# Performance work log

Hardware: AMD Instinct MI355X
Metric: run time of the kernel (lower is better)

## Reference

```python
import jax, jax.numpy as jnp
import numpy as np

N_NODES = 100000


def _graph_conv(x, W, b, src, dst, deg_out, deg_in, relu):
    # DGL GraphConv, norm='both':
    #   h = (x * D_out^{-1/2}) W ; agg = scatter_sum over edges ; out = agg * D_in^{-1/2} + b
    norm_src = jax.lax.rsqrt(jnp.maximum(deg_out, 1.0))  # [N]
    norm_dst = jax.lax.rsqrt(jnp.maximum(deg_in, 1.0))   # [N]
    h = (x * norm_src[:, None]) @ W                       # [N, d_out]
    agg = jax.ops.segment_sum(h[src], dst, num_segments=N_NODES)  # [N, d_out]
    out = agg * norm_dst[:, None] + b
    return jax.nn.relu(out) if relu else out


def setup_inputs() -> dict:
    key = jax.random.key(0)
    ks = jax.random.split(key, 8)
    E = 1600000
    in_dim, hid_dim, out_dim = 128, 128, 64
    feat = jax.random.normal(ks[0], (N_NODES, in_dim), dtype=jnp.float32)
    edge_index = jax.random.randint(ks[1], (2, E), 0, N_NODES, dtype=jnp.int64)
    s = 1.0 / np.sqrt(in_dim)
    sh = 1.0 / np.sqrt(hid_dim)
    return {
        "feat": feat,
        "edge_index": edge_index,
        "W0": jax.random.normal(ks[2], (in_dim, hid_dim), dtype=jnp.float32) * s,
        "b0": jnp.zeros((hid_dim,), dtype=jnp.float32),
        "W1": jax.random.normal(ks[3], (hid_dim, hid_dim), dtype=jnp.float32) * sh,
        "b1": jnp.zeros((hid_dim,), dtype=jnp.float32),
        "W2": jax.random.normal(ks[4], (hid_dim, out_dim), dtype=jnp.float32) * sh,
        "b2": jnp.zeros((out_dim,), dtype=jnp.float32),
    }


def reference(feat, edge_index, W0, b0, W1, b1, W2, b2):
    src, dst = edge_index[0], edge_index[1]
    ones = jnp.ones(src.shape, dtype=feat.dtype)
    deg_out = jax.ops.segment_sum(ones, src, num_segments=N_NODES)  # src out-degree
    deg_in = jax.ops.segment_sum(ones, dst, num_segments=N_NODES)   # dst in-degree
    h = _graph_conv(feat, W0, b0, src, dst, deg_out, deg_in, relu=True)
    h = _graph_conv(h, W1, b1, src, dst, deg_out, deg_in, relu=True)
    h = _graph_conv(h, W2, b2, src, dst, deg_out, deg_in, relu=False)
    return h
```

## Files before the change

kernel.cpp:

```cpp
#include <hip/hip_runtime.h>
#include <hip/hip_fp16.h>


typedef _Float16 h8 __attribute__((ext_vector_type(8)));
typedef float f32x4 __attribute__((ext_vector_type(4)));

#define HWORDS 25024
#define NHIST 32

__global__ __launch_bounds__(256) void k_pre(const int* __restrict__ src, int E,
                                             unsigned* __restrict__ histo,
                                             int* __restrict__ deg_i, int n,
                                             const float* __restrict__ W0,
                                             const float* __restrict__ W1,
                                             const float* __restrict__ W2,
                                             __half* __restrict__ Wt0,
                                             __half* __restrict__ Wt1,
                                             __half* __restrict__ Wt2) {
    __shared__ unsigned H[HWORDS];
    const int b = blockIdx.x;
    if (b < NHIST) {
        for (int i = threadIdx.x; i < HWORDS; i += 256) H[i] = 0;
        __syncthreads();
        const int perB = ((E + NHIST - 1) / NHIST + 3) & ~3;
        const int e0 = b * perB, e1 = min(e0 + perB, E);
        int i = e0 + threadIdx.x * 4;
        for (; i + 3 < e1; i += 1024) {
            int4 s4 = *(const int4*)(src + i);
            atomicAdd(&H[s4.x >> 2], 1u << ((s4.x & 3) * 8));
            atomicAdd(&H[s4.y >> 2], 1u << ((s4.y & 3) * 8));
            atomicAdd(&H[s4.z >> 2], 1u << ((s4.z & 3) * 8));
            atomicAdd(&H[s4.w >> 2], 1u << ((s4.w & 3) * 8));
        }
        for (; i < e1; ++i) {
            int s = src[i];
            atomicAdd(&H[s >> 2], 1u << ((s & 3) * 8));
        }
        __syncthreads();
        unsigned* outp = histo + b * HWORDS;
        for (int i2 = threadIdx.x; i2 < HWORDS; i2 += 256) outp[i2] = H[i2];
    } else if (b < NHIST + 8) {
        int per = (n + 7) / 8;
        int s0 = (b - NHIST) * per, s1 = min(s0 + per, n);
        for (int i = s0 + threadIdx.x; i < s1; i += 256) deg_i[i] = 0;
    } else {
        int j0 = (b - NHIST - 8) * 20480;
        for (int j = j0 + threadIdx.x; j < j0 + 20480; j += 256) {
            if (j < 16384) {
                int nn = j >> 7, k = j & 127;
                Wt0[j] = __float2half(W0[k * 128 + nn]);
            } else if (j < 32768) {
                int i2 = j - 16384;
                int nn = i2 >> 7, k = i2 & 127;
                Wt1[i2] = __float2half(W1[k * 128 + nn]);
            } else if (j < 40960) {
                int i2 = j - 32768;
                int nn = i2 >> 7, k = i2 & 127;
                Wt2[i2] = __float2half(W2[k * 64 + nn]);
            }
        }
    }
}

template <int BN, bool F32A>
__device__ __forceinline__ void gemm_body(const void* __restrict__ Ap,
                                          const __half* __restrict__ Wt,
                                          __half* __restrict__ C, int n, int gb) {
    constexpr int K = 128, BM = 128, LDR = K + 8;
    __shared__ __half Al[BM * LDR];
    __shared__ __half Bl[BN * LDR];
    const int tid = threadIdx.x;
    const int row0 = gb * BM;
    if (F32A) {
        const float* A = (const float*)Ap;
#pragma unroll
        for (int q = 0; q < 16; ++q) {
            int fi = q * 256 + tid;
            int r = fi >> 5, c = (fi & 31) * 4;
            int gr = row0 + r;
            float4 v = make_float4(0.f, 0.f, 0.f, 0.f);
            if (gr < n) v = *(const float4*)(A + (size_t)gr * K + c);
            __half2 h0 = __floats2half2_rn(v.x, v.y);
            __half2 h1 = __floats2half2_rn(v.z, v.w);
            uint2 pk = make_uint2(*(unsigned*)&h0, *(unsigned*)&h1);
            *(uint2*)&Al[r * LDR + c] = pk;
        }
    } else {
        const __half* A = (const __half*)Ap;
#pragma unroll
        for (int q = 0; q < 8; ++q) {
            int fi = q * 256 + tid;
            int r = fi >> 4, c = (fi & 15) * 8;
            int gr = row0 + r;
            float4 v = make_float4(0.f, 0.f, 0.f, 0.f);
            if (gr < n) v = *(const float4*)(A + (size_t)gr * K + c);
            *(float4*)&Al[r * LDR + c] = v;
        }
    }
#pragma unroll
    for (int q = 0; q < BN / 16; ++q) {
        int fi = q * 256 + tid;
        int r = fi >> 4, c = (fi & 15) * 8;
        *(float4*)&Bl[r * LDR + c] = *(const float4*)(Wt + (size_t)r * K + c);
    }
    __syncthreads();
    const int wid = tid >> 6, lane = tid & 63;
    const int lo = lane & 15, hi = lane >> 4;
    constexpr int NC = BN / 16;
    f32x4 acc[2][NC];
#pragma unroll
    for (int t = 0; t < 2; ++t)
#pragma unroll
        for (int c = 0; c < NC; ++c) acc[t][c] = (f32x4){0.f, 0.f, 0.f, 0.f};
#pragma unroll
    for (int kc = 0; kc < 4; ++kc) {
        h8 aF[2];
#pragma unroll
        for (int t = 0; t < 2; ++t)
            aF[t] = *(const h8*)&Al[(32 * wid + 16 * t + lo) * LDR + 32 * kc + 8 * hi];
#pragma unroll
        for (int c = 0; c < NC; ++c) {
            h8 bF = *(const h8*)&Bl[(16 * c + lo) * LDR + 32 * kc + 8 * hi];
#pragma unroll
            for (int t = 0; t < 2; ++t)
                acc[t][c] = __builtin_amdgcn_mfma_f32_16x16x32_f16(aF[t], bF, acc[t][c], 0, 0, 0);
        }
    }
#pragma unroll
    for (int t = 0; t < 2; ++t) {
#pragma unroll
        for (int j = 0; j < 4; ++j) {
            int gr = row0 + 32 * wid + 16 * t + 4 * hi + j;
            if (gr < n) {
#pragma unroll
                for (int c = 0; c < NC; ++c)
                    C[(size_t)gr * BN + 16 * c + lo] = __float2half(acc[t][c][j]);
            }
        }
    }
}

__global__ __launch_bounds__(256) void k_fused0(
        const float* __restrict__ feat, const __half* __restrict__ Wt0,
        __half* __restrict__ Hu, int n,
        const int* __restrict__ dst, int E,
        int* __restrict__ deg_i, int* __restrict__ pos,
        int CB, int T) {
    const int b = blockIdx.x;
    const long lo = (long)b * CB / T, hi = (long)(b + 1) * CB / T;
    if (hi > lo) {
        int i = (int)lo * 256 + threadIdx.x;
        const int stride = CB * 256;
        for (; i < E; i += stride) {
            pos[i] = atomicAdd(&deg_i[dst[i]], 1);
        }
    } else {
        gemm_body<128, true>(feat, Wt0, Hu, n, b - (int)lo);
    }
}

template <int BN>
__global__ __launch_bounds__(256) void k_gemm(const __half* __restrict__ X,
                                              const __half* __restrict__ Wt,
                                              __half* __restrict__ C, int n) {
    gemm_body<BN, false>(X, Wt, C, n, blockIdx.x);
}

__global__ __launch_bounds__(256) void k_scan1(const int* __restrict__ deg_i,
                                               const unsigned* __restrict__ histo,
                                               int* __restrict__ rp,
                                               int* __restrict__ bsum,
                                               float* __restrict__ ns,
                                               float* __restrict__ nd, int n) {
    const int tid = threadIdx.x, lane = tid & 63, wid = tid >> 6;
    int i = blockIdx.x * 256 + tid;
    int v = (i < n) ? deg_i[i] : 0;
    if (i < n) {
        nd[i] = rsqrtf((float)max(v, 1));
        int w = i >> 2, sh = (i & 3) * 8;
        int dgo = 0;
#pragma unroll
        for (int b = 0; b < NHIST; ++b)
            dgo += (histo[b * HWORDS + w] >> sh) & 255u;
        ns[i] = rsqrtf((float)max(dgo, 1));
    }
    int x = v;
#pragma unroll
    for (int off = 1; off < 64; off <<= 1) {
        int t = __shfl_up(x, off, 64);
        if (lane >= off) x += t;
    }
    __shared__ int ws[4];
    if (lane == 63) ws[wid] = x;
    __syncthreads();
    int wo = 0;
    for (int k = 0; k < wid; ++k) wo += ws[k];
    int incl = wo + x;
    if (i < n) rp[i] = incl - v;
    if (tid == 255) bsum[blockIdx.x] = incl;
}

__global__ __launch_bounds__(512) void k_scan2(int* __restrict__ bsum, int nb,
                                               int* __restrict__ rpN) {
    __shared__ int s[512];
    const int tid = threadIdx.x;
    int v = (tid < nb) ? bsum[tid] : 0;
    s[tid] = v;
    __syncthreads();
    for (int off = 1; off < 512; off <<= 1) {
        int t = (tid >= off) ? s[tid - off] : 0;
        __syncthreads();
        s[tid] += t;
        __syncthreads();
    }
    if (tid < nb) bsum[tid] = s[tid] - v;
    if (tid == nb - 1) *rpN = v;
}

__global__ void k_scatter(const int* __restrict__ src, const int* __restrict__ dst, int E,
                          const int* __restrict__ rp, const int* __restrict__ bsum,
                          const int* __restrict__ pos, int* __restrict__ csr) {
    int i = blockIdx.x * blockDim.x + threadIdx.x;
    int stride = gridDim.x * blockDim.x;
    for (; i < E; i += stride) {
        int d = dst[i];
        csr[rp[d] + bsum[d >> 8] + pos[i]] = src[i];
    }
}

template <bool RELU, bool SSCALE>
__global__ __launch_bounds__(256) void k_agg128h(const __half2* __restrict__ H,
                                                 const int* __restrict__ rp,
                                                 const int* __restrict__ bsum,
                                                 const int* __restrict__ cs,
                                                 const float* __restrict__ nd,
                                                 const float* __restrict__ ns,
                                                 const float* __restrict__ b,
                                                 __half2* __restrict__ out, int n) {
    const int wid = threadIdx.x >> 6, lane = threadIdx.x & 63;
    const int node = blockIdx.x * 4 + wid;
    if (node >= n) return;
    const int beg = rp[node] + bsum[node >> 8];
    const int end = rp[node + 1] + bsum[(node + 1) >> 8];
    float2 a0 = make_float2(0.f, 0.f), a1 = a0, a2 = a0, a3 = a0;
    float2 a4 = a0, a5 = a0, a6 = a0, a7 = a0;
    for (int e = beg; e < end; e += 8) {
        int s[8];
        float w[8];
#pragma unroll
        for (int j = 0; j < 8; ++j) {
            int idx = e + j;
            int r = (idx < end) ? idx : beg;
            r = __builtin_amdgcn_readfirstlane(r);
            s[j] = cs[r];
            w[j] = (idx < end) ? 1.f : 0.f;
        }
        if (SSCALE) {
#pragma unroll
            for (int j = 0; j < 8; ++j) w[j] *= ns[s[j]];
        }
        float2 v0 = __half22float2(H[(size_t)s[0] * 64 + lane]);
        float2 v1 = __half22float2(H[(size_t)s[1] * 64 + lane]);
        float2 v2 = __half22float2(H[(size_t)s[2] * 64 + lane]);
        float2 v3 = __half22float2(H[(size_t)s[3] * 64 + lane]);
        float2 v4 = __half22float2(H[(size_t)s[4] * 64 + lane]);
        float2 v5 = __half22float2(H[(size_t)s[5] * 64 + lane]);
        float2 v6 = __half22float2(H[(size_t)s[6] * 64 + lane]);
        float2 v7 = __half22float2(H[(size_t)s[7] * 64 + lane]);
        a0.x = fmaf(v0.x, w[0], a0.x); a0.y = fmaf(v0.y, w[0], a0.y);
        a1.x = fmaf(v1.x, w[1], a1.x); a1.y = fmaf(v1.y, w[1], a1.y);
        a2.x = fmaf(v2.x, w[2], a2.x); a2.y = fmaf(v2.y, w[2], a2.y);
        a3.x = fmaf(v3.x, w[3], a3.x); a3.y = fmaf(v3.y, w[3], a3.y);
        a4.x = fmaf(v4.x, w[4], a4.x); a4.y = fmaf(v4.y, w[4], a4.y);
        a5.x = fmaf(v5.x, w[5], a5.x); a5.y = fmaf(v5.y, w[5], a5.y);
        a6.x = fmaf(v6.x, w[6], a6.x); a6.y = fmaf(v6.y, w[6], a6.y);
        a7.x = fmaf(v7.x, w[7], a7.x); a7.y = fmaf(v7.y, w[7], a7.y);
    }
    const float sc = nd[node];
    const float sn = ns[node];
    float2 bb = ((const float2*)b)[lane];
    float ax = ((a0.x + a1.x) + (a2.x + a3.x)) + ((a4.x + a5.x) + (a6.x + a7.x));
    float ay = ((a0.y + a1.y) + (a2.y + a3.y)) + ((a4.y + a5.y) + (a6.y + a7.y));
    float ox = ax * sc + bb.x;
    float oy = ay * sc + bb.y;
    if (RELU) { ox = fmaxf(ox, 0.f); oy = fmaxf(oy, 0.f); }
    ox *= sn; oy *= sn;
    out[(size_t)node * 64 + lane] = __floats2half2_rn(ox, oy);
}

__global__ __launch_bounds__(256) void k_agg64h(const __half* __restrict__ H,
                                                const int* __restrict__ rp,
                                                const int* __restrict__ bsum,
                                                const int* __restrict__ cs,
                                                const float* __restrict__ nd,
                                                const float* __restrict__ b,
                                                float* __restrict__ out, int n) {
    const int wid = threadIdx.x >> 6, lane = threadIdx.x & 63;
    const int node = blockIdx.x * 4 + wid;
    if (node >= n) return;
    const int beg = rp[node] + bsum[node >> 8];
    const int end = rp[node + 1] + bsum[(node + 1) >> 8];
    float a0 = 0.f, a1 = 0.f, a2 = 0.f, a3 = 0.f;
    float a4 = 0.f, a5 = 0.f, a6 = 0.f, a7 = 0.f;
    for (int e = beg; e < end; e += 8) {
        int s[8];
        float w[8];
#pragma unroll
        for (int j = 0; j < 8; ++j) {
            int idx = e + j;
            int r = (idx < end) ? idx : beg;
            r = __builtin_amdgcn_readfirstlane(r);
            s[j] = cs[r];
            w[j] = (idx < end) ? 1.f : 0.f;
        }
        a0 = fmaf(__half2float(H[(size_t)s[0] * 64 + lane]), w[0], a0);
        a1 = fmaf(__half2float(H[(size_t)s[1] * 64 + lane]), w[1], a1);
        a2 = fmaf(__half2float(H[(size_t)s[2] * 64 + lane]), w[2], a2);
        a3 = fmaf(__half2float(H[(size_t)s[3] * 64 + lane]), w[3], a3);
        a4 = fmaf(__half2float(H[(size_t)s[4] * 64 + lane]), w[4], a4);
        a5 = fmaf(__half2float(H[(size_t)s[5] * 64 + lane]), w[5], a5);
        a6 = fmaf(__half2float(H[(size_t)s[6] * 64 + lane]), w[6], a6);
        a7 = fmaf(__half2float(H[(size_t)s[7] * 64 + lane]), w[7], a7);
    }
    float a = ((a0 + a1) + (a2 + a3)) + ((a4 + a5) + (a6 + a7));
    out[(size_t)node * 64 + lane] = a * nd[node] + b[lane];
}

extern "C" void kernel_launch(void* const* d_in, const int* in_sizes, int n_in,
                              void* d_out, int out_size, void* d_ws, size_t ws_size,
                              hipStream_t stream) {
    const float* feat = (const float*)d_in[0];
    const int* ei = (const int*)d_in[1];
    const float* W0 = (const float*)d_in[2];
    const float* b0 = (const float*)d_in[3];
    const float* W1 = (const float*)d_in[4];
    const float* b1 = (const float*)d_in[5];
    const float* W2 = (const float*)d_in[6];
    const float* b2 = (const float*)d_in[7];
    float* out = (float*)d_out;

    const int N = in_sizes[0] / 128;
    const int E = in_sizes[1] / 2;
    const int* src = ei;
    const int* dst = ei + E;
    const int NB = (N + 255) / 256;

    char* w = (char*)d_ws;
    float* norm_src = (float*)w; w += (size_t)N * 4;
    float* norm_dst = (float*)w; w += (size_t)N * 4;
    int* deg_i = (int*)w;        w += (size_t)N * 4;
    unsigned* histo = (unsigned*)w; w += (size_t)NHIST * HWORDS * 4;
    int* rp    = (int*)w;        w += ((size_t)(N + 1) * 4 + 15) / 16 * 16;
    int* bsum  = (int*)w;        w += 512 * 4;
    int* pos   = (int*)w;        w += (size_t)E * 4;
    int* csr   = (int*)w;        w += (size_t)E * 4;
    __half* Wt0 = (__half*)w;    w += 128 * 128 * 2;
    __half* Wt1 = (__half*)w;    w += 128 * 128 * 2;
    __half* Wt2 = (__half*)w;    w += 128 * 64 * 2;
    __half* Hb = (__half*)w;     w += (size_t)N * 128 * 2;
    __half* Xb = (__half*)w;     w += (size_t)N * 128 * 2;

    const int GB = (N + 127) / 128;
    const int CB = 1024;
    const int T = GB + CB;

    k_pre<<<NHIST + 8 + 2, 256, 0, stream>>>(src, E, histo, deg_i, N,
                                             W0, W1, W2, Wt0, Wt1, Wt2);
    k_fused0<<<T, 256, 0, stream>>>(feat, Wt0, Hb, N, dst, E, deg_i, pos, CB, T);
    k_scan1<<<NB, 256, 0, stream>>>(deg_i, histo, rp, bsum, norm_src, norm_dst, N);
    k_scan2<<<1, 512, 0, stream>>>(bsum, NB, rp + N);
    k_scatter<<<2048, 256, 0, stream>>>(src, dst, E, rp, bsum, pos, csr);

    const int agg_grid = (N + 3) / 4;
    k_agg128h<true, true><<<agg_grid, 256, 0, stream>>>((const __half2*)Hb, rp, bsum, csr,
                                                        norm_dst, norm_src, b0, (__half2*)Xb, N);
    k_gemm<128><<<GB, 256, 0, stream>>>(Xb, Wt1, Hb, N);
    k_agg128h<true, false><<<agg_grid, 256, 0, stream>>>((const __half2*)Hb, rp, bsum, csr,
                                                         norm_dst, norm_src, b1, (__half2*)Xb, N);
    k_gemm<64><<<GB, 256, 0, stream>>>(Xb, Wt2, Hb, N);
    k_agg64h<<<agg_grid, 256, 0, stream>>>(Hb, rp, bsum, csr, norm_dst, b2, out, N);
}
```

Measured before the change: 370.5 us.

## Build CSR via per-chunk LDS dst histograms instead of global atomics

Replaces the global-atomic in-degree count and per-edge position array with per-chunk shared-memory histograms of dst, which are prefix-summed across chunks in the scan kernel. A new scatter kernel recomputes each edge's slot using LDS atomics against the chunk prefix, which removes the pos buffer and the global atomic traffic. The first GEMM is no longer fused with the counting pass and runs as a separate launch. The aggregation loops are unrolled from 8 to 16 edges to put more gathers in flight. The risks are 8-bit packed counters overflowing if a node gets 256 or more edges in one chunk, and only 64 blocks doing the scatter.

After: 392.1 us. 1.06x slower.

```diff
diff --git a/kernel.cpp b/kernel.cpp
--- a/kernel.cpp
+++ b/kernel.cpp
@@ -6,11 +6,13 @@
 typedef float f32x4 __attribute__((ext_vector_type(4)));
 
 #define HWORDS 25024
-#define NHIST 32
-
-__global__ __launch_bounds__(256) void k_pre(const int* __restrict__ src, int E,
-                                             unsigned* __restrict__ histo,
-                                             int* __restrict__ deg_i, int n,
+#define NHS 32
+#define NHD 64
+
+__global__ __launch_bounds__(256) void k_pre(const int* __restrict__ src,
+                                             const int* __restrict__ dst, int E,
+                                             unsigned* __restrict__ histo_s,
+                                             unsigned* __restrict__ histo_d,
                                              const float* __restrict__ W0,
                                              const float* __restrict__ W1,
                                              const float* __restrict__ W2,
@@ -19,32 +21,32 @@
                                              __half* __restrict__ Wt2) {
     __shared__ unsigned H[HWORDS];
     const int b = blockIdx.x;
-    if (b < NHIST) {
+    if (b < NHS + NHD) {
+        const bool isS = b < NHS;
+        const int c = isS ? b : b - NHS;
+        const int NC = isS ? NHS : NHD;
+        const int* arr = isS ? src : dst;
+        unsigned* outp = (isS ? histo_s : histo_d) + (size_t)c * HWORDS;
         for (int i = threadIdx.x; i < HWORDS; i += 256) H[i] = 0;
         __syncthreads();
-        const int perB = ((E + NHIST - 1) / NHIST + 3) & ~3;
-        const int e0 = b * perB, e1 = min(e0 + perB, E);
+        const int perB = ((E + NC - 1) / NC + 3) & ~3;
+        const int e0 = c * perB, e1 = min(e0 + perB, E);
         int i = e0 + threadIdx.x * 4;
         for (; i + 3 < e1; i += 1024) {
-            int4 s4 = *(const int4*)(src + i);
+            int4 s4 = *(const int4*)(arr + i);
             atomicAdd(&H[s4.x >> 2], 1u << ((s4.x & 3) * 8));
             atomicAdd(&H[s4.y >> 2], 1u << ((s4.y & 3) * 8));
             atomicAdd(&H[s4.z >> 2], 1u << ((s4.z & 3) * 8));
             atomicAdd(&H[s4.w >> 2], 1u << ((s4.w & 3) * 8));
         }
         for (; i < e1; ++i) {
-            int s = src[i];
+            int s = arr[i];
             atomicAdd(&H[s >> 2], 1u << ((s & 3) * 8));
         }
         __syncthreads();
-        unsigned* outp = histo + b * HWORDS;
         for (int i2 = threadIdx.x; i2 < HWORDS; i2 += 256) outp[i2] = H[i2];
-    } else if (b < NHIST + 8) {
-        int per = (n + 7) / 8;
-        int s0 = (b - NHIST) * per, s1 = min(s0 + per, n);
-        for (int i = s0 + threadIdx.x; i < s1; i += 256) deg_i[i] = 0;
     } else {
-        int j0 = (b - NHIST - 8) * 20480;
+        int j0 = (b - NHS - NHD) * 20480;
         for (int j = j0 + threadIdx.x; j < j0 + 20480; j += 256) {
             if (j < 16384) {
                 int nn = j >> 7, k = j & 127;
@@ -62,126 +64,38 @@
     }
 }
 
-template <int BN, bool F32A>
-__device__ __forceinline__ void gemm_body(const void* __restrict__ Ap,
-                                          const __half* __restrict__ Wt,
-                                          __half* __restrict__ C, int n, int gb) {
-    constexpr int K = 128, BM = 128, LDR = K + 8;
-    __shared__ __half Al[BM * LDR];
-    __shared__ __half Bl[BN * LDR];
-    const int tid = threadIdx.x;
-    const int row0 = gb * BM;
-    if (F32A) {
-        const float* A = (const float*)Ap;
-#pragma unroll
-        for (int q = 0; q < 16; ++q) {
-            int fi = q * 256 + tid;
-            int r = fi >> 5, c = (fi & 31) * 4;
-            int gr = row0 + r;
-            float4 v = make_float4(0.f, 0.f, 0.f, 0.f);
-            if (gr < n) v = *(const float4*)(A + (size_t)gr * K + c);
-            __half2 h0 = __floats2half2_rn(v.x, v.y);
-            __half2 h1 = __floats2half2_rn(v.z, v.w);
-            uint2 pk = make_uint2(*(unsigned*)&h0, *(unsigned*)&h1);
-            *(uint2*)&Al[r * LDR + c] = pk;
-        }
-    } else {
-        const __half* A = (const __half*)Ap;
-#pragma unroll
-        for (int q = 0; q < 8; ++q) {
-            int fi = q * 256 + tid;
-            int r = fi >> 4, c = (fi & 15) * 8;
-            int gr = row0 + r;
-            float4 v = make_float4(0.f, 0.f, 0.f, 0.f);
-            if (gr < n) v = *(const float4*)(A + (size_t)gr * K + c);
-            *(float4*)&Al[r * LDR + c] = v;
-        }
-    }
-#pragma unroll
-    for (int q = 0; q < BN / 16; ++q) {
-        int fi = q * 256 + tid;
-        int r = fi >> 4, c = (fi & 15) * 8;
-        *(float4*)&Bl[r * LDR + c] = *(const float4*)(Wt + (size_t)r * K + c);
-    }
-    __syncthreads();
-    const int wid = tid >> 6, lane = tid & 63;
-    const int lo = lane & 15, hi = lane >> 4;
-    constexpr int NC = BN / 16;
-    f32x4 acc[2][NC];
-#pragma unroll
-    for (int t = 0; t < 2; ++t)
-#pragma unroll
-        for (int c = 0; c < NC; ++c) acc[t][c] = (f32x4){0.f, 0.f, 0.f, 0.f};
-#pragma unroll
-    for (int kc = 0; kc < 4; ++kc) {
-        h8 aF[2];
-#pragma unroll
-        for (int t = 0; t < 2; ++t)
-            aF[t] = *(const h8*)&Al[(32 * wid + 16 * t + lo) * LDR + 32 * kc + 8 * hi];
-#pragma unroll
-        for (int c = 0; c < NC; ++c) {
-            h8 bF = *(const h8*)&Bl[(16 * c + lo) * LDR + 32 * kc + 8 * hi];
-#pragma unroll
-            for (int t = 0; t < 2; ++t)
-                acc[t][c] = __builtin_amdgcn_mfma_f32_16x16x32_f16(aF[t], bF, acc[t][c], 0, 0, 0);
-        }
-    }
-#pragma unroll
-    for (int t = 0; t < 2; ++t) {
-#pragma unroll
-        for (int j = 0; j < 4; ++j) {
-            int gr = row0 + 32 * wid + 16 * t + 4 * hi + j;
-            if (gr < n) {
-#pragma unroll
-                for (int c = 0; c < NC; ++c)
-                    C[(size_t)gr * BN + 16 * c + lo] = __float2half(acc[t][c][j]);
-            }
-        }
-    }
-}
-
-__global__ __launch_bounds__(256) void k_fused0(
-        const float* __restrict__ feat, const __half* __restrict__ Wt0,
-        __half* __restrict__ Hu, int n,
-        const int* __restrict__ dst, int E,
-        int* __restrict__ deg_i, int* __restrict__ pos,
-        int CB, int T) {
-    const int b = blockIdx.x;
-    const long lo = (long)b * CB / T, hi = (long)(b + 1) * CB / T;
-    if (hi > lo) {
-        int i = (int)lo * 256 + threadIdx.x;
-        const int stride = CB * 256;
-        for (; i < E; i += stride) {
-            pos[i] = atomicAdd(&deg_i[dst[i]], 1);
-        }
-    } else {
-        gemm_body<128, true>(feat, Wt0, Hu, n, b - (int)lo);
-    }
-}
-
-template <int BN>
-__global__ __launch_bounds__(256) void k_gemm(const __half* __restrict__ X,
-                                              const __half* __restrict__ Wt,
-                                              __half* __restrict__ C, int n) {
-    gemm_body<BN, false>(X, Wt, C, n, blockIdx.x);
-}
-
-__global__ __launch_bounds__(256) void k_scan1(const int* __restrict__ deg_i,
-                                               const unsigned* __restrict__ histo,
+__global__ __launch_bounds__(256) void k_scan1(const unsigned* __restrict__ histo_s,
+                                               unsigned* __restrict__ histo_d,
                                                int* __restrict__ rp,
                                                int* __restrict__ bsum,
                                                float* __restrict__ ns,
                                                float* __restrict__ nd, int n) {
+    __shared__ unsigned di4[64];
+    __shared__ unsigned do4[64];
     const int tid = threadIdx.x, lane = tid & 63, wid = tid >> 6;
+    if (tid < 64) {
+        const int w = blockIdx.x * 64 + tid;
+        unsigned run4 = 0;
+#pragma unroll
+        for (int b = 0; b < NHD; ++b) {
+            unsigned c4 = histo_d[(size_t)b * HWORDS + w];
+            histo_d[(size_t)b * HWORDS + w] = run4;
+            run4 += c4;
+        }
+        di4[tid] = run4;
+        unsigned s4 = 0;
+#pragma unroll
+        for (int b = 0; b < NHS; ++b) s4 += histo_s[(size_t)b * HWORDS + w];
+        do4[tid] = s4;
+    }
+    __syncthreads();
     int i = blockIdx.x * 256 + tid;
-    int v = (i < n) ? deg_i[i] : 0;
+    int v = 0;
     if (i < n) {
+        int sh = (tid & 3) * 8;
+        v = (di4[tid >> 2] >> sh) & 255;
+        int dgo = (do4[tid >> 2] >> sh) & 255;
         nd[i] = rsqrtf((float)max(v, 1));
-        int w = i >> 2, sh = (i & 3) * 8;
-        int dgo = 0;
-#pragma unroll
-        for (int b = 0; b < NHIST; ++b)
-            dgo += (histo[b * HWORDS + w] >> sh) & 255u;
         ns[i] = rsqrtf((float)max(dgo, 1));
     }
     int x = v;
@@ -217,15 +131,120 @@
     if (tid == nb - 1) *rpN = v;
 }
 
-__global__ void k_scatter(const int* __restrict__ src, const int* __restrict__ dst, int E,
-                          const int* __restrict__ rp, const int* __restrict__ bsum,
-                          const int* __restrict__ pos, int* __restrict__ csr) {
-    int i = blockIdx.x * blockDim.x + threadIdx.x;
-    int stride = gridDim.x * blockDim.x;
-    for (; i < E; i += stride) {
-        int d = dst[i];
-        csr[rp[d] + bsum[d >> 8] + pos[i]] = src[i];
-    }
+__global__ __launch_bounds__(256) void k_scatter2(const int* __restrict__ src,
+                                                  const int* __restrict__ dst, int E,
+                                                  const int* __restrict__ rp,
+                                                  const int* __restrict__ bsum,
+                                                  const unsigned* __restrict__ pfx_all,
+                                                  int* __restrict__ csr) {
+    __shared__ unsigned Hd[HWORDS];
+    for (int i = threadIdx.x; i < HWORDS; i += 256) Hd[i] = 0;
+    __syncthreads();
+    const int c = blockIdx.x;
+    const int perB = ((E + NHD - 1) / NHD + 3) & ~3;
+    const int e0 = c * perB, e1 = min(e0 + perB, E);
+    const unsigned* pfx = pfx_all + (size_t)c * HWORDS;
+    int i = e0 + threadIdx.x * 4;
+    for (; i + 3 < e1; i += 1024) {
+        int4 d4 = *(const int4*)(dst + i);
+        int4 s4 = *(const int4*)(src + i);
+#define PROC(dd, ss)                                                            \
+        {                                                                       \
+            int sh = ((dd) & 3) * 8;                                            \
+            int base = rp[dd] + bsum[(dd) >> 8] +                               \
+                       (int)((pfx[(dd) >> 2] >> sh) & 255u);                    \
+            unsigned old = atomicAdd(&Hd[(dd) >> 2], 1u << sh);                 \
+            csr[base + (int)((old >> sh) & 255u)] = (ss);                       \
+        }
+        PROC(d4.x, s4.x) PROC(d4.y, s4.y) PROC(d4.z, s4.z) PROC(d4.w, s4.w)
+    }
+    for (; i < e1; ++i) PROC(dst[i], src[i])
+#undef PROC
+}
+
+template <int BN, bool F32A>
+__device__ __forceinline__ void gemm_body(const void* __restrict__ Ap,
+                                          const __half* __restrict__ Wt,
+                                          __half* __restrict__ C, int n, int gb) {
+    constexpr int K = 128, BM = 128, LDR = K + 8;
+    __shared__ __half Al[BM * LDR];
+    __shared__ __half Bl[BN * LDR];
+    const int tid = threadIdx.x;
+    const int row0 = gb * BM;
+    if (F32A) {
+        const float* A = (const float*)Ap;
+#pragma unroll
+        for (int q = 0; q < 16; ++q) {
+            int fi = q * 256 + tid;
+            int r = fi >> 5, c = (fi & 31) * 4;
+            int gr = row0 + r;
+            float4 v = make_float4(0.f, 0.f, 0.f, 0.f);
+            if (gr < n) v = *(const float4*)(A + (size_t)gr * K + c);
+            __half2 h0 = __floats2half2_rn(v.x, v.y);
+            __half2 h1 = __floats2half2_rn(v.z, v.w);
+            uint2 pk = make_uint2(*(unsigned*)&h0, *(unsigned*)&h1);
+            *(uint2*)&Al[r * LDR + c] = pk;
+        }
+    } else {
+        const __half* A = (const __half*)Ap;
+#pragma unroll
+        for (int q = 0; q < 8; ++q) {
+            int fi = q * 256 + tid;
+            int r = fi >> 4, c = (fi & 15) * 8;
+            int gr = row0 + r;
+            float4 v = make_float4(0.f, 0.f, 0.f, 0.f);
+            if (gr < n) v = *(const float4*)(A + (size_t)gr * K + c);
+            *(float4*)&Al[r * LDR + c] = v;
+        }
+    }
+#pragma unroll
+    for (int q = 0; q < BN / 16; ++q) {
+        int fi = q * 256 + tid;
+        int r = fi >> 4, c = (fi & 15) * 8;
+        *(float4*)&Bl[r * LDR + c] = *(const float4*)(Wt + (size_t)r * K + c);
+    }
+    __syncthreads();
+    const int wid = tid >> 6, lane = tid & 63;
+    const int lo = lane & 15, hi = lane >> 4;
+    constexpr int NC = BN / 16;
+    f32x4 acc[2][NC];
+#pragma unroll
+    for (int t = 0; t < 2; ++t)
+#pragma unroll
+        for (int c = 0; c < NC; ++c) acc[t][c] = (f32x4){0.f, 0.f, 0.f, 0.f};
+#pragma unroll
+    for (int kc = 0; kc < 4; ++kc) {
+        h8 aF[2];
+#pragma unroll
+        for (int t = 0; t < 2; ++t)
+            aF[t] = *(const h8*)&Al[(32 * wid + 16 * t + lo) * LDR + 32 * kc + 8 * hi];
+#pragma unroll
+        for (int c = 0; c < NC; ++c) {
+            h8 bF = *(const h8*)&Bl[(16 * c + lo) * LDR + 32 * kc + 8 * hi];
+#pragma unroll
+            for (int t = 0; t < 2; ++t)
+                acc[t][c] = __builtin_amdgcn_mfma_f32_16x16x32_f16(aF[t], bF, acc[t][c], 0, 0, 0);
+        }
+    }
+#pragma unroll
+    for (int t = 0; t < 2; ++t) {
+#pragma unroll
+        for (int j = 0; j < 4; ++j) {
+            int gr = row0 + 32 * wid + 16 * t + 4 * hi + j;
+            if (gr < n) {
+#pragma unroll
+                for (int c = 0; c < NC; ++c)
+                    C[(size_t)gr * BN + 16 * c + lo] = __float2half(acc[t][c][j]);
+            }
+        }
+    }
+}
+
+template <int BN, bool F32A>
+__global__ __launch_bounds__(256) void k_gemm(const void* __restrict__ A,
+                                              const __half* __restrict__ Wt,
+                                              __half* __restrict__ C, int n) {
+    gemm_body<BN, F32A>(A, Wt, C, n, blockIdx.x);
 }
 
 template <bool RELU, bool SSCALE>
@@ -244,11 +263,11 @@
     const int end = rp[node + 1] + bsum[(node + 1) >> 8];
     float2 a0 = make_float2(0.f, 0.f), a1 = a0, a2 = a0, a3 = a0;
     float2 a4 = a0, a5 = a0, a6 = a0, a7 = a0;
-    for (int e = beg; e < end; e += 8) {
-        int s[8];
-        float w[8];
-#pragma unroll
-        for (int j = 0; j < 8; ++j) {
+    for (int e = beg; e < end; e += 16) {
+        int s[16];
+        float w[16];
+#pragma unroll
+        for (int j = 0; j < 16; ++j) {
             int idx = e + j;
             int r = (idx < end) ? idx : beg;
             r = __builtin_amdgcn_readfirstlane(r);
@@ -257,24 +276,28 @@
         }
         if (SSCALE) {
 #pragma unroll
-            for (int j = 0; j < 8; ++j) w[j] *= ns[s[j]];
-        }
-        float2 v0 = __half22float2(H[(size_t)s[0] * 64 + lane]);
-        float2 v1 = __half22float2(H[(size_t)s[1] * 64 + lane]);
-        float2 v2 = __half22float2(H[(size_t)s[2] * 64 + lane]);
-        float2 v3 = __half22float2(H[(size_t)s[3] * 64 + lane]);
-        float2 v4 = __half22float2(H[(size_t)s[4] * 64 + lane]);
-        float2 v5 = __half22float2(H[(size_t)s[5] * 64 + lane]);
-        float2 v6 = __half22float2(H[(size_t)s[6] * 64 + lane]);
-        float2 v7 = __half22float2(H[(size_t)s[7] * 64 + lane]);
-        a0.x = fmaf(v0.x, w[0], a0.x); a0.y = fmaf(v0.y, w[0], a0.y);
-        a1.x = fmaf(v1.x, w[1], a1.x); a1.y = fmaf(v1.y, w[1], a1.y);
-        a2.x = fmaf(v2.x, w[2], a2.x); a2.y = fmaf(v2.y, w[2], a2.y);
-        a3.x = fmaf(v3.x, w[3], a3.x); a3.y = fmaf(v3.y, w[3], a3.y);
-        a4.x = fmaf(v4.x, w[4], a4.x); a4.y = fmaf(v4.y, w[4], a4.y);
-        a5.x = fmaf(v5.x, w[5], a5.x); a5.y = fmaf(v5.y, w[5], a5.y);
-        a6.x = fmaf(v6.x, w[6], a6.x); a6.y = fmaf(v6.y, w[6], a6.y);
-        a7.x = fmaf(v7.x, w[7], a7.x); a7.y = fmaf(v7.y, w[7], a7.y);
+            for (int j = 0; j < 16; ++j) w[j] *= ns[s[j]];
+        }
+        float2 v[16];
+#pragma unroll
+        for (int j = 0; j < 16; ++j)
+            v[j] = __half22float2(H[(size_t)s[j] * 64 + lane]);
+        a0.x = fmaf(v[0].x, w[0], fmaf(v[8].x, w[8], a0.x));
+        a0.y = fmaf(v[0].y, w[0], fmaf(v[8].y, w[8], a0.y));
+        a1.x = fmaf(v[1].x, w[1], fmaf(v[9].x, w[9], a1.x));
+        a1.y = fmaf(v[1].y, w[1], fmaf(v[9].y, w[9], a1.y));
+        a2.x = fmaf(v[2].x, w[2], fmaf(v[10].x, w[10], a2.x));
+        a2.y = fmaf(v[2].y, w[2], fmaf(v[10].y, w[10], a2.y));
+        a3.x = fmaf(v[3].x, w[3], fmaf(v[11].x, w[11], a3.x));
+        a3.y = fmaf(v[3].y, w[3], fmaf(v[11].y, w[11], a3.y));
+        a4.x = fmaf(v[4].x, w[4], fmaf(v[12].x, w[12], a4.x));
+        a4.y = fmaf(v[4].y, w[4], fmaf(v[12].y, w[12], a4.y));
+        a5.x = fmaf(v[5].x, w[5], fmaf(v[13].x, w[13], a5.x));
+        a5.y = fmaf(v[5].y, w[5], fmaf(v[13].y, w[13], a5.y));
+        a6.x = fmaf(v[6].x, w[6], fmaf(v[14].x, w[14], a6.x));
+        a6.y = fmaf(v[6].y, w[6], fmaf(v[14].y, w[14], a6.y));
+        a7.x = fmaf(v[7].x, w[7], fmaf(v[15].x, w[15], a7.x));
+        a7.y = fmaf(v[7].y, w[7], fmaf(v[15].y, w[15], a7.y));
     }
     const float sc = nd[node];
     const float sn = ns[node];
@@ -302,25 +325,29 @@
     const int end = rp[node + 1] + bsum[(node + 1) >> 8];
     float a0 = 0.f, a1 = 0.f, a2 = 0.f, a3 = 0.f;
     float a4 = 0.f, a5 = 0.f, a6 = 0.f, a7 = 0.f;
-    for (int e = beg; e < end; e += 8) {
-        int s[8];
-        float w[8];
-#pragma unroll
-        for (int j = 0; j < 8; ++j) {
+    for (int e = beg; e < end; e += 16) {
+        int s[16];
+        float w[16];
+#pragma unroll
+        for (int j = 0; j < 16; ++j) {
             int idx = e + j;
             int r = (idx < end) ? idx : beg;
             r = __builtin_amdgcn_readfirstlane(r);
             s[j] = cs[r];
             w[j] = (idx < end) ? 1.f : 0.f;
         }
-        a0 = fmaf(__half2float(H[(size_t)s[0] * 64 + lane]), w[0], a0);
-        a1 = fmaf(__half2float(H[(size_t)s[1] * 64 + lane]), w[1], a1);
-        a2 = fmaf(__half2float(H[(size_t)s[2] * 64 + lane]), w[2], a2);
-        a3 = fmaf(__half2float(H[(size_t)s[3] * 64 + lane]), w[3], a3);
-        a4 = fmaf(__half2float(H[(size_t)s[4] * 64 + lane]), w[4], a4);
-        a5 = fmaf(__half2float(H[(size_t)s[5] * 64 + lane]), w[5], a5);
-        a6 = fmaf(__half2float(H[(size_t)s[6] * 64 + lane]), w[6], a6);
-        a7 = fmaf(__half2float(H[(size_t)s[7] * 64 + lane]), w[7], a7);
+        float v[16];
+#pragma unroll
+        for (int j = 0; j < 16; ++j)
+            v[j] = __half2float(H[(size_t)s[j] * 64 + lane]);
+        a0 = fmaf(v[0], w[0], fmaf(v[8], w[8], a0));
+        a1 = fmaf(v[1], w[1], fmaf(v[9], w[9], a1));
+        a2 = fmaf(v[2], w[2], fmaf(v[10], w[10], a2));
+        a3 = fmaf(v[3], w[3], fmaf(v[11], w[11], a3));
+        a4 = fmaf(v[4], w[4], fmaf(v[12], w[12], a4));
+        a5 = fmaf(v[5], w[5], fmaf(v[13], w[13], a5));
+        a6 = fmaf(v[6], w[6], fmaf(v[14], w[14], a6));
+        a7 = fmaf(v[7], w[7], fmaf(v[15], w[15], a7));
     }
     float a = ((a0 + a1) + (a2 + a3)) + ((a4 + a5) + (a6 + a7));
     out[(size_t)node * 64 + lane] = a * nd[node] + b[lane];
@@ -348,11 +375,10 @@
     char* w = (char*)d_ws;
     float* norm_src = (float*)w; w += (size_t)N * 4;
     float* norm_dst = (float*)w; w += (size_t)N * 4;
-    int* deg_i = (int*)w;        w += (size_t)N * 4;
-    unsigned* histo = (unsigned*)w; w += (size_t)NHIST * HWORDS * 4;
+    unsigned* histo_s = (unsigned*)w; w += (size_t)NHS * HWORDS * 4;
+    unsigned* histo_d = (unsigned*)w; w += (size_t)NHD * HWORDS * 4;
     int* rp    = (int*)w;        w += ((size_t)(N + 1) * 4 + 15) / 16 * 16;
     int* bsum  = (int*)w;        w += 512 * 4;
-    int* pos   = (int*)w;        w += (size_t)E * 4;
     int* csr   = (int*)w;        w += (size_t)E * 4;
     __half* Wt0 = (__half*)w;    w += 128 * 128 * 2;
     __half* Wt1 = (__half*)w;    w += 128 * 128 * 2;
@@ -361,22 +387,20 @@
     __half* Xb = (__half*)w;     w += (size_t)N * 128 * 2;
 
     const int GB = (N + 127) / 128;
-    const int CB = 1024;
-    const int T = GB + CB;
-
-    k_pre<<<NHIST + 8 + 2, 256, 0, stream>>>(src, E, histo, deg_i, N,
+    const int agg_grid = (N + 3) / 4;
+
+    k_pre<<<NHS + NHD + 2, 256, 0, stream>>>(src, dst, E, histo_s, histo_d,
                                              W0, W1, W2, Wt0, Wt1, Wt2);
-    k_fused0<<<T, 256, 0, stream>>>(feat, Wt0, Hb, N, dst, E, deg_i, pos, CB, T);
-    k_scan1<<<NB, 256, 0, stream>>>(deg_i, histo, rp, bsum, norm_src, norm_dst, N);
+    k_scan1<<<NB, 256, 0, stream>>>(histo_s, histo_d, rp, bsum, norm_src, norm_dst, N);
     k_scan2<<<1, 512, 0, stream>>>(bsum, NB, rp + N);
-    k_scatter<<<2048, 256, 0, stream>>>(src, dst, E, rp, bsum, pos, csr);
-
-    const int agg_grid = (N + 3) / 4;
+    k_scatter2<<<NHD, 256, 0, stream>>>(src, dst, E, rp, bsum, histo_d, csr);
+
+    k_gemm<128, true><<<GB, 256, 0, stream>>>(feat, Wt0, Hb, N);
     k_agg128h<true, true><<<agg_grid, 256, 0, stream>>>((const __half2*)Hb, rp, bsum, csr,
                                                         norm_dst, norm_src, b0, (__half2*)Xb, N);
-    k_gemm<128><<<GB, 256, 0, stream>>>(Xb, Wt1, Hb, N);
+    k_gemm<128, false><<<GB, 256, 0, stream>>>(Xb, Wt1, Hb, N);
     k_agg128h<true, false><<<agg_grid, 256, 0, stream>>>((const __half2*)Hb, rp, bsum, csr,
                                                          norm_dst, norm_src, b1, (__half2*)Xb, N);
-    k_gemm<64><<<GB, 256, 0, stream>>>(Xb, Wt2, Hb, N);
+    k_gemm<64, false><<<GB, 256, 0, stream>>>(Xb, Wt2, Hb, N);
     k_agg64h<<<agg_grid, 256, 0, stream>>>(Hb, rp, bsum, csr, norm_dst, b2, out, N);
 }
```
